# Kernel tuning notes

Hardware: AMD Instinct MI355X
Metric: run time of the kernel (lower is better)

The kernel has to match this reference:

```python
import jax, jax.numpy as jnp
import numpy as np

B, L, H, S = 16, 2048, 1024, 32
P, N_ASP, N_RAT = 256, 8, 5


def _layernorm(x, scale, bias, eps=1e-5):
    mu = jnp.mean(x, axis=-1, keepdims=True)
    var = jnp.mean(jnp.square(x - mu), axis=-1, keepdims=True)
    return (x - mu) * jax.lax.rsqrt(var + eps) * scale + bias


def _bndl(x, ln_s, ln_b, W):
    # BnDropLin eval: LayerNorm -> (Dropout off) -> Linear(no bias)
    return _layernorm(x, ln_s, ln_b) @ W


def setup_inputs() -> dict:
    key = jax.random.key(0)
    ks = jax.random.split(key, 8)
    outputs = jax.random.normal(ks[0], (B, L, H), dtype=jnp.float32)
    mask = jnp.ones((B, L), dtype=jnp.float32)
    # p_index: binary sentence-boundary markers, exactly S per doc, min gap 2
    rng = np.random.default_rng(0)
    p = np.zeros((B, L), dtype=np.int32)
    for b in range(B):
        idx = np.sort(rng.choice(L // 2 - 1, size=S, replace=False)) * 2 + 1
        p[b, idx] = 1
    p_index = jnp.asarray(p)
    sc = 0.02
    params = dict(
        ln_a_s=jnp.ones((H,), jnp.float32), ln_a_b=jnp.zeros((H,), jnp.float32),
        W_a=jax.random.normal(ks[1], (H, P), jnp.float32) * sc,
        ln_s_s=jnp.ones((H,), jnp.float32), ln_s_b=jnp.zeros((H,), jnp.float32),
        W_s=jax.random.normal(ks[2], (H, P), jnp.float32) * sc,
        ln_asp_s=jnp.ones((P,), jnp.float32), ln_asp_b=jnp.zeros((P,), jnp.float32),
        W_asp=jax.random.normal(ks[3], (P, N_ASP + 1), jnp.float32) * sc,
        ln_se_s=jnp.ones((P,), jnp.float32), ln_se_b=jnp.zeros((P,), jnp.float32),
        W_se=jax.random.normal(ks[4], (P, N_RAT), jnp.float32) * sc,
    )
    return dict(outputs=outputs, mask=mask, p_index=p_index, n_sent=S, **params)


def _segment_means(proj, end, start):
    # proj: [B, L, P]; start/end: [B, S] token index ranges [start, end)
    c = jnp.concatenate([jnp.zeros_like(proj[:, :1]), jnp.cumsum(proj, axis=1)], axis=1)  # [B,L+1,P]
    s_end = jnp.take_along_axis(c, end[:, :, None], axis=1)
    s_beg = jnp.take_along_axis(c, start[:, :, None], axis=1)
    cnt = (end - start).astype(proj.dtype)[:, :, None]
    return (s_end - s_beg) / cnt  # [B, S, P]


def reference(outputs, mask, p_index, n_sent,
              ln_a_s, ln_a_b, W_a, ln_s_s, ln_s_b, W_s,
              ln_asp_s, ln_asp_b, W_asp, ln_se_s, ln_se_b, W_se):
    b, l, h = outputs.shape
    n_asp = W_asp.shape[1] - 1
    flat = outputs.reshape(-1, h)
    a_proj = jax.nn.gelu(_bndl(flat, ln_a_s, ln_a_b, W_a), approximate=False).reshape(b, l, -1)
    s_proj = jax.nn.gelu(_bndl(flat, ln_s_s, ln_s_b, W_s), approximate=False).reshape(b, l, -1)
    # sentence boundaries: positions of nonzeros (exactly n_sent per row)
    pos = jnp.where(p_index > 0, jnp.arange(l)[None, :], l)
    pi = jnp.sort(pos, axis=1)[:, :n_sent]                      # [B,S] boundary idx (exclusive end)
    start = jnp.concatenate([jnp.zeros_like(pi[:, :1]), pi[:, :-1] + 1], axis=1)
    a_sent = _segment_means(a_proj, pi, start)                  # [B,S,P]
    s_sent = _segment_means(s_proj, pi, start)                  # [B,S,P]
    a_flat = a_sent.reshape(b * n_sent, -1)
    s_flat = s_sent.reshape(b * n_sent, -1)
    aspect_dist = jax.nn.softmax(_bndl(a_flat, ln_asp_s, ln_asp_b, W_asp), axis=1)  # [N, n_asp+1]
    aw = aspect_dist[:, :n_asp]                                 # [N, n_asp]
    sent_bmm = aw[:, :, None] * s_flat[:, None, :]              # [N, n_asp, P]
    doc_sum = sent_bmm.reshape(b, n_sent, n_asp, -1).sum(axis=1)        # [B, n_asp, P]
    w_sum = aw.reshape(b, n_sent, n_asp).sum(axis=1)[:, :, None]        # [B, n_asp, 1]
    doc_emb = doc_sum / w_sum
    # shared sentiment head (ModuleList([m]*n_asp) aliases one module)
    result = _bndl(doc_emb, ln_se_s, ln_se_b, W_se)             # [B, n_asp, n_rat]
    aspect_doc = aspect_dist.reshape(b, n_sent, n_asp + 1)
    return (result, outputs, aspect_doc)
```

## Files before the change

### kernel.cpp

```cpp
#include <hip/hip_runtime.h>
#include <cstdint>
#include <cstddef>

#define B_   16
#define L_   2048
#define H_   1024
#define S_   32
#define P_   256
#define NASP 8
#define NRAT 5
#define M_   (B_*L_)
#define N_   (2*P_)

typedef unsigned short u16;
typedef __bf16 bf16;
typedef u16  u16x4  __attribute__((ext_vector_type(4)));
typedef u16  u16x8  __attribute__((ext_vector_type(8)));
typedef bf16 bf16x8 __attribute__((ext_vector_type(8)));
typedef float f32x4 __attribute__((ext_vector_type(4)));

__device__ __forceinline__ u16 f2b(float f){
  unsigned int u = __float_as_uint(f);
  u += 0x7FFFu + ((u >> 16) & 1u);
  return (u16)(u >> 16);
}
__device__ __forceinline__ float b2f(u16 v){
  return __uint_as_float(((unsigned int)v) << 16);
}

__device__ __forceinline__ void gload_lds16(const u16* g, u16* l){
  __builtin_amdgcn_global_load_lds(
      (const __attribute__((address_space(1))) unsigned int*)g,
      (__attribute__((address_space(3))) unsigned int*)l, 16, 0, 0);
}

__device__ __forceinline__ float2 block_reduce2(float a, float b){
  __shared__ float sh[8];
  #pragma unroll
  for (int o = 32; o > 0; o >>= 1){
    a += __shfl_down(a, o, 64);
    b += __shfl_down(b, o, 64);
  }
  int w = threadIdx.x >> 6;
  if ((threadIdx.x & 63) == 0){ sh[w] = a; sh[w + 4] = b; }
  __syncthreads();
  float2 r;
  r.x = sh[0] + sh[1] + sh[2] + sh[3];
  r.y = sh[4] + sh[5] + sh[6] + sh[7];
  __syncthreads();
  return r;
}

__global__ void fold_k(const float* __restrict__ Wa, const float* __restrict__ Ws,
                       const float* __restrict__ sa, const float* __restrict__ ba,
                       const float* __restrict__ ss, const float* __restrict__ bs,
                       u16* __restrict__ WcT, float* __restrict__ biasc){
  int n = blockIdx.x;
  const float* W; const float* sc; const float* bi; int col;
  if (n < P_){ W = Wa; sc = sa; bi = ba; col = n; }
  else       { W = Ws; sc = ss; bi = bs; col = n - P_; }
  float bacc = 0.f;
  #pragma unroll
  for (int i = 0; i < 4; ++i){
    int k = threadIdx.x + i * 256;
    float w = W[(size_t)k * P_ + col];
    WcT[(size_t)n * H_ + k] = f2b(w * sc[k]);
    bacc += w * bi[k];
  }
  float2 r = block_reduce2(bacc, 0.f);
  if (threadIdx.x == 0) biasc[n] = r.x;
}

__global__ void markers_k(const int* __restrict__ p_index, int* __restrict__ pi){
  int b = blockIdx.x;
  int lane = threadIdx.x;
  int cnt = 0;
  for (int c = 0; c < L_ / 64; ++c){
    int pos = c * 64 + lane;
    bool f = p_index[(size_t)b * L_ + pos] > 0;
    unsigned long long m = __ballot(f);
    int before = __popcll(m & ((1ull << lane) - 1ull));
    if (f){
      int idx = cnt + before;
      if (idx < S_) pi[b * S_ + idx] = pos;
    }
    cnt += __popcll(m);
  }
}

template<bool FUSE_ECHO>
__global__ void stats_xhat_k(const float* __restrict__ x, u16* __restrict__ xhat,
                             float4* __restrict__ echo){
  int row = blockIdx.x;
  int t = threadIdx.x;
  float4 v = ((const float4*)(x + (size_t)row * H_))[t];
  if (FUSE_ECHO) echo[(size_t)row * (H_ / 4) + t] = v;
  float s  = v.x + v.y + v.z + v.w;
  float ss = v.x*v.x + v.y*v.y + v.z*v.z + v.w*v.w;
  float2 r = block_reduce2(s, ss);
  float mean = r.x * (1.f / H_);
  float var  = fmaxf(r.y * (1.f / H_) - mean * mean, 0.f);
  float rstd = rsqrtf(var + 1e-5f);
  u16x4 o;
  o[0] = f2b((v.x - mean) * rstd);
  o[1] = f2b((v.y - mean) * rstd);
  o[2] = f2b((v.z - mean) * rstd);
  o[3] = f2b((v.w - mean) * rstd);
  ((u16x4*)(xhat + (size_t)row * H_))[t] = o;
}

#define NT_ 16
__global__ __launch_bounds__(512, 2) void gemm_k(const u16* __restrict__ xhat,
                                                 const u16* __restrict__ WcT,
                                                 const float* __restrict__ biasc,
                                                 u16* __restrict__ proj){
  __shared__ __align__(16) u16 As[2][256 * 64];
  __shared__ __align__(16) u16 Bs[2][256 * 64];
  int t = threadIdx.x;
  unsigned int l = blockIdx.x;
  unsigned int xcd  = l & 7;
  unsigned int slot = l >> 3;
  int nbase = (int)(slot & 1) * 256;
  int mbase = (int)(xcd * 16 + (slot >> 1)) * 256;

  int w = t >> 6, lane = t & 63;
  int wr = w >> 2, wc = w & 3;
  int quad = lane >> 4, l15 = lane & 15;

  int rin = lane >> 3;
  int g = (lane & 7) ^ rin;
  const u16* gA[4]; const u16* gB[4]; int off[4];
  #pragma unroll
  for (int i = 0; i < 4; ++i){
    int r = w * 32 + i * 8 + rin;
    gA[i] = xhat + (size_t)(mbase + r) * H_ + g * 8;
    gB[i] = WcT  + (size_t)(nbase + r) * H_ + g * 8;
    off[i] = (w * 4 + i) * 512;
  }

  f32x4 acc[8][4] = {};

#define STAGE_(buf, tile) do{ int kk_ = (tile) * 64;            \
    gload_lds16(gA[0] + kk_, &As[buf][off[0]]);                 \
    gload_lds16(gA[1] + kk_, &As[buf][off[1]]);                 \
    gload_lds16(gA[2] + kk_, &As[buf][off[2]]);                 \
    gload_lds16(gA[3] + kk_, &As[buf][off[3]]);                 \
    gload_lds16(gB[0] + kk_, &Bs[buf][off[0]]);                 \
    gload_lds16(gB[1] + kk_, &Bs[buf][off[1]]);                 \
    gload_lds16(gB[2] + kk_, &Bs[buf][off[2]]);                 \
    gload_lds16(gB[3] + kk_, &Bs[buf][off[3]]);                 \
  }while(0)

  STAGE_(0, 0);
  STAGE_(1, 1);
  asm volatile("s_waitcnt vmcnt(8)" ::: "memory");
  __builtin_amdgcn_sched_barrier(0);
  __builtin_amdgcn_s_barrier();

  for (int kt = 0; kt < NT_; ++kt){
    int cur = kt & 1;
    __builtin_amdgcn_s_setprio(1);
    #pragma unroll
    for (int s = 0; s < 2; ++s){
      bf16x8 af[8], bfr[4];
      #pragma unroll
      for (int im = 0; im < 8; ++im){
        int R = wr * 128 + im * 16 + l15;
        int c = (s * 4 + quad) ^ (R & 7);
        af[im] = *reinterpret_cast<const bf16x8*>(&As[cur][R * 64 + c * 8]);
      }
      #pragma unroll
      for (int in = 0; in < 4; ++in){
        int R = wc * 64 + in * 16 + l15;
        int c = (s * 4 + quad) ^ (R & 7);
        bfr[in] = *reinterpret_cast<const bf16x8*>(&Bs[cur][R * 64 + c * 8]);
      }
      #pragma unroll
      for (int im = 0; im < 8; ++im)
        #pragma unroll
        for (int in = 0; in < 4; ++in)
          acc[im][in] = __builtin_amdgcn_mfma_f32_16x16x32_bf16(af[im], bfr[in], acc[im][in], 0, 0, 0);
    }
    __builtin_amdgcn_s_setprio(0);
    if (kt == NT_ - 1) break;
    __builtin_amdgcn_s_barrier();
    if (kt + 2 < NT_){
      STAGE_(cur, kt + 2);
      asm volatile("s_waitcnt vmcnt(8)" ::: "memory");
    } else {
      asm volatile("s_waitcnt vmcnt(0)" ::: "memory");
    }
    __builtin_amdgcn_sched_barrier(0);
    __builtin_amdgcn_s_barrier();
  }
#undef STAGE_

  #pragma unroll
  for (int in = 0; in < 4; ++in){
    int col = nbase + wc * 64 + in * 16 + l15;
    float bv = biasc[col];
    #pragma unroll
    for (int im = 0; im < 8; ++im){
      #pragma unroll
      for (int r = 0; r < 4; ++r){
        int rowg = mbase + wr * 128 + im * 16 + quad * 4 + r;
        float vv = acc[im][in][r] + bv;
        float gl = 0.5f * vv * (1.0f + erff(vv * 0.70710678118654752f));
        proj[(size_t)rowg * N_ + col] = f2b(gl);
      }
    }
  }
}

__global__ __launch_bounds__(1024) void segmean_k(const u16* __restrict__ proj,
                                                  const int* __restrict__ pi,
                                                  float* __restrict__ sent){
  int b = blockIdx.x, j = blockIdx.y;
  int t = threadIdx.x;
  int rg   = t >> 6;
  int lane = t & 63;
  int end   = pi[b * S_ + j];
  int start = (j == 0) ? 0 : (pi[b * S_ + j - 1] + 1);
  end   = min(max(end, 0), L_);
  start = min(max(start, 0), end);
  int cnt = max(end - start, 1);
  float inv = 1.0f / (float)cnt;

  float s[8] = {};
  const u16* base = proj + ((size_t)b * L_ + start) * N_ + lane * 8;
  for (int r = rg; r < cnt; r += 16){
    u16x8 v = *reinterpret_cast<const u16x8*>(base + (size_t)r * N_);
    #pragma unroll
    for (int k = 0; k < 8; ++k) s[k] += b2f(v[k]);
  }

  __shared__ float sh[16][N_];
  #pragma unroll
  for (int k = 0; k < 8; ++k) sh[rg][lane * 8 + k] = s[k];
  __syncthreads();

  if (t < N_){
    float acc = 0.f;
    #pragma unroll
    for (int g = 0; g < 16; ++g) acc += sh[g][t];
    sent[((size_t)b * S_ + j) * N_ + t] = acc * inv;
  }
}

__global__ void aspect_k(const float* __restrict__ sent,
                         const float* __restrict__ lns, const float* __restrict__ lnb,
                         const float* __restrict__ Wasp,
                         float* __restrict__ out_adoc, float* __restrict__ aw){
  int sidx = blockIdx.x;
  int t = threadIdx.x;
  float a = sent[(size_t)sidx * N_ + t];
  float2 r = block_reduce2(a, a * a);
  float mean = r.x * (1.f / P_);
  float var  = fmaxf(r.y * (1.f / P_) - mean * mean, 0.f);
  float rstd = rsqrtf(var + 1e-5f);
  __shared__ float shv[P_];
  shv[t] = (a - mean) * rstd * lns[t] + lnb[t];
  __syncthreads();
  __shared__ float lg[NASP + 1];
  if (t < NASP + 1){
    float acc = 0.f;
    for (int p = 0; p < P_; ++p) acc += shv[p] * Wasp[p * (NASP + 1) + t];
    lg[t] = acc;
  }
  __syncthreads();
  __shared__ float pr[NASP + 1];
  if (t == 0){
    float m = lg[0];
    #pragma unroll
    for (int i = 1; i < NASP + 1; ++i) m = fmaxf(m, lg[i]);
    float s = 0.f;
    #pragma unroll
    for (int i = 0; i < NASP + 1; ++i){ float e = expf(lg[i] - m); pr[i] = e; s += e; }
    float is = 1.f / s;
    #pragma unroll
    for (int i = 0; i < NASP + 1; ++i) pr[i] *= is;
  }
  __syncthreads();
  if (t < NASP + 1) out_adoc[(size_t)sidx * (NASP + 1) + t] = pr[t];
  if (t < NASP)     aw[(size_t)sidx * NASP + t] = pr[t];
}

__global__ void result_k(const float* __restrict__ sent, const float* __restrict__ aw,
                         const float* __restrict__ lns, const float* __restrict__ lnb,
                         const float* __restrict__ Wse, float* __restrict__ out){
  int ba = blockIdx.x;
  int b = ba >> 3, a = ba & 7;
  int t = threadIdx.x;
  float acc = 0.f, wsum = 0.f;
  for (int s2 = 0; s2 < S_; ++s2){
    float w = aw[((size_t)(b * S_ + s2)) * NASP + a];
    acc  += w * sent[((size_t)(b * S_ + s2)) * N_ + P_ + t];
    wsum += w;
  }
  float d = acc / fmaxf(wsum, 1e-20f);
  float2 r = block_reduce2(d, d * d);
  float mean = r.x * (1.f / P_);
  float var  = fmaxf(r.y * (1.f / P_) - mean * mean, 0.f);
  float rstd = rsqrtf(var + 1e-5f);
  __shared__ float shv[P_];
  shv[t] = (d - mean) * rstd * lns[t] + lnb[t];
  __syncthreads();
  if (t < NRAT){
    float s = 0.f;
    for (int p = 0; p < P_; ++p) s += shv[p] * Wse[p * NRAT + t];
    out[(size_t)ba * NRAT + t] = s;
  }
}

__global__ void copy_k(const float4* __restrict__ src, float4* __restrict__ dst){
  size_t i = (size_t)blockIdx.x * 256 + threadIdx.x;
  dst[i] = src[i];
}

extern "C" void kernel_launch(void* const* d_in, const int* in_sizes, int n_in,
                              void* d_out, int out_size, void* d_ws, size_t ws_size,
                              hipStream_t stream) {
  const float* x        = (const float*)d_in[0];
  const int*   p_index  = (const int*)d_in[2];
  const float* ln_a_s   = (const float*)d_in[4];
  const float* ln_a_b   = (const float*)d_in[5];
  const float* W_a      = (const float*)d_in[6];
  const float* ln_s_s   = (const float*)d_in[7];
  const float* ln_s_b   = (const float*)d_in[8];
  const float* W_s      = (const float*)d_in[9];
  const float* ln_asp_s = (const float*)d_in[10];
  const float* ln_asp_b = (const float*)d_in[11];
  const float* W_asp    = (const float*)d_in[12];
  const float* ln_se_s  = (const float*)d_in[13];
  const float* ln_se_b  = (const float*)d_in[14];
  const float* W_se     = (const float*)d_in[15];

  float* out_result = (float*)d_out;
  float* out_echo   = out_result + 640;
  float* out_adoc   = out_echo + (size_t)M_ * H_;

  char* ws = (char*)d_ws;
  u16*   WcT   = (u16*)ws;   ws += (size_t)N_ * H_ * 2;
  float* biasc = (float*)ws; ws += (size_t)N_ * 4;
  int*   pi    = (int*)ws;   ws += (size_t)B_ * S_ * 4;
  float* sent  = (float*)ws; ws += (size_t)B_ * S_ * N_ * 4;
  float* aw    = (float*)ws; ws += (size_t)B_ * S_ * NASP * 4;

  size_t small_used = (size_t)(ws - (char*)d_ws);
  size_t big_need   = small_used + (size_t)M_ * N_ * 2 + (size_t)M_ * H_ * 2;
  bool   big_ws     = ws_size >= big_need;

  u16* proj; u16* xhat;
  if (big_ws){
    proj = (u16*)ws;
    xhat = proj + (size_t)M_ * N_;
  } else {
    proj = (u16*)out_echo;
    xhat = proj + (size_t)M_ * N_;
  }

  fold_k<<<N_, 256, 0, stream>>>(W_a, W_s, ln_a_s, ln_a_b, ln_s_s, ln_s_b, WcT, biasc);
  markers_k<<<B_, 64, 0, stream>>>(p_index, pi);
  if (big_ws)
    stats_xhat_k<true ><<<M_, 256, 0, stream>>>(x, xhat, (float4*)out_echo);
  else
    stats_xhat_k<false><<<M_, 256, 0, stream>>>(x, xhat, nullptr);
  gemm_k<<<256, 512, 0, stream>>>(xhat, WcT, biasc, proj);
  segmean_k<<<dim3(B_, S_), 1024, 0, stream>>>(proj, pi, sent);
  aspect_k<<<B_ * S_, 256, 0, stream>>>(sent, ln_asp_s, ln_asp_b, W_asp, out_adoc, aw);
  result_k<<<B_ * NASP, 256, 0, stream>>>(sent, aw, ln_se_s, ln_se_b, W_se, out_result);
  if (!big_ws)
    copy_k<<<(M_ * H_ / 4) / 256, 256, 0, stream>>>((const float4*)x, (float4*)out_echo);
}
```

Before: 393.5 us.

## Restructure GEMM main loop into four barrier-synced phases with interleaved prefetch

The GEMM k-loop now prefetches only one tile ahead instead of two. The global-to-LDS loads are split into four chunks, each issued alongside one of four LDS-read/MFMA phases, with block barriers between phases. The aim is to spread memory traffic evenly and keep the waves in lockstep, in the style of ping-pong scheduling. The s_setprio calls are dropped. Separately, the xhat and WcT stores are switched to nontemporal stores. The extra barriers and the shallower prefetch may expose more latency.

```diff
diff --git a/kernel.cpp b/kernel.cpp
--- a/kernel.cpp
+++ b/kernel.cpp
@@ -64,7 +64,7 @@
   for (int i = 0; i < 4; ++i){
     int k = threadIdx.x + i * 256;
     float w = W[(size_t)k * P_ + col];
-    WcT[(size_t)n * H_ + k] = f2b(w * sc[k]);
+    __builtin_nontemporal_store(f2b(w * sc[k]), &WcT[(size_t)n * H_ + k]);
     bacc += w * bi[k];
   }
   float2 r = block_reduce2(bacc, 0.f);
@@ -106,7 +106,7 @@
   o[1] = f2b((v.y - mean) * rstd);
   o[2] = f2b((v.z - mean) * rstd);
   o[3] = f2b((v.w - mean) * rstd);
-  ((u16x4*)(xhat + (size_t)row * H_))[t] = o;
+  __builtin_nontemporal_store(o, (u16x4*)(xhat + (size_t)row * H_) + t);
 }
 
 #define NT_ 16
@@ -140,60 +140,76 @@
 
   f32x4 acc[8][4] = {};
 
-#define STAGE_(buf, tile) do{ int kk_ = (tile) * 64;            \
-    gload_lds16(gA[0] + kk_, &As[buf][off[0]]);                 \
-    gload_lds16(gA[1] + kk_, &As[buf][off[1]]);                 \
-    gload_lds16(gA[2] + kk_, &As[buf][off[2]]);                 \
-    gload_lds16(gA[3] + kk_, &As[buf][off[3]]);                 \
-    gload_lds16(gB[0] + kk_, &Bs[buf][off[0]]);                 \
-    gload_lds16(gB[1] + kk_, &Bs[buf][off[1]]);                 \
-    gload_lds16(gB[2] + kk_, &Bs[buf][off[2]]);                 \
-    gload_lds16(gB[3] + kk_, &Bs[buf][off[3]]);                 \
-  }while(0)
-
-  STAGE_(0, 0);
-  STAGE_(1, 1);
-  asm volatile("s_waitcnt vmcnt(8)" ::: "memory");
+  #pragma unroll
+  for (int i = 0; i < 4; ++i){
+    gload_lds16(gA[i], &As[0][off[i]]);
+    gload_lds16(gB[i], &Bs[0][off[i]]);
+  }
+  asm volatile("s_waitcnt vmcnt(0)" ::: "memory");
   __builtin_amdgcn_sched_barrier(0);
   __builtin_amdgcn_s_barrier();
 
+#define LDA8(dst, S, IM) { int R_ = wr*128 + (IM)*16 + l15;                  \
+    int c_ = ((S)*4+quad) ^ (R_ & 7);                                        \
+    dst = *reinterpret_cast<const bf16x8*>(&As[cur][R_*64 + c_*8]); }
+#define LDB8(dst, S, IN) { int R_ = wc*64 + (IN)*16 + l15;                   \
+    int c_ = ((S)*4+quad) ^ (R_ & 7);                                        \
+    dst = *reinterpret_cast<const bf16x8*>(&Bs[cur][R_*64 + c_*8]); }
+#define PHASE_WAIT  __builtin_amdgcn_s_barrier();                            \
+    asm volatile("s_waitcnt lgkmcnt(0)" ::: "memory");                       \
+    __builtin_amdgcn_sched_barrier(0);
+#define MM4(AV, I)                                                           \
+    acc[I][0] = __builtin_amdgcn_mfma_f32_16x16x32_bf16(AV, b0, acc[I][0], 0,0,0); \
+    acc[I][1] = __builtin_amdgcn_mfma_f32_16x16x32_bf16(AV, b1, acc[I][1], 0,0,0); \
+    acc[I][2] = __builtin_amdgcn_mfma_f32_16x16x32_bf16(AV, b2, acc[I][2], 0,0,0); \
+    acc[I][3] = __builtin_amdgcn_mfma_f32_16x16x32_bf16(AV, b3, acc[I][3], 0,0,0);
+
   for (int kt = 0; kt < NT_; ++kt){
-    int cur = kt & 1;
-    __builtin_amdgcn_s_setprio(1);
-    #pragma unroll
-    for (int s = 0; s < 2; ++s){
-      bf16x8 af[8], bfr[4];
-      #pragma unroll
-      for (int im = 0; im < 8; ++im){
-        int R = wr * 128 + im * 16 + l15;
-        int c = (s * 4 + quad) ^ (R & 7);
-        af[im] = *reinterpret_cast<const bf16x8*>(&As[cur][R * 64 + c * 8]);
-      }
-      #pragma unroll
-      for (int in = 0; in < 4; ++in){
-        int R = wc * 64 + in * 16 + l15;
-        int c = (s * 4 + quad) ^ (R & 7);
-        bfr[in] = *reinterpret_cast<const bf16x8*>(&Bs[cur][R * 64 + c * 8]);
-      }
-      #pragma unroll
-      for (int im = 0; im < 8; ++im)
-        #pragma unroll
-        for (int in = 0; in < 4; ++in)
-          acc[im][in] = __builtin_amdgcn_mfma_f32_16x16x32_bf16(af[im], bfr[in], acc[im][in], 0, 0, 0);
+    int cur = kt & 1, nxt = cur ^ 1;
+    int kk1 = (kt + 1) * 64;
+    bool pf = (kt + 1 < NT_);
+    bf16x8 a0, a1, a2, a3, b0, b1, b2, b3;
+
+    LDB8(b0,0,0); LDB8(b1,0,1); LDB8(b2,0,2); LDB8(b3,0,3);
+    LDA8(a0,0,0); LDA8(a1,0,1); LDA8(a2,0,2); LDA8(a3,0,3);
+    if (pf){ gload_lds16(gA[0]+kk1, &As[nxt][off[0]]);
+             gload_lds16(gA[1]+kk1, &As[nxt][off[1]]); }
+    PHASE_WAIT;
+    MM4(a0,0) MM4(a1,1) MM4(a2,2) MM4(a3,3)
+    __builtin_amdgcn_s_barrier();
+
+    LDA8(a0,0,4); LDA8(a1,0,5); LDA8(a2,0,6); LDA8(a3,0,7);
+    if (pf){ gload_lds16(gA[2]+kk1, &As[nxt][off[2]]);
+             gload_lds16(gA[3]+kk1, &As[nxt][off[3]]); }
+    PHASE_WAIT;
+    MM4(a0,4) MM4(a1,5) MM4(a2,6) MM4(a3,7)
+    __builtin_amdgcn_s_barrier();
+
+    LDB8(b0,1,0); LDB8(b1,1,1); LDB8(b2,1,2); LDB8(b3,1,3);
+    LDA8(a0,1,0); LDA8(a1,1,1); LDA8(a2,1,2); LDA8(a3,1,3);
+    if (pf){ gload_lds16(gB[0]+kk1, &Bs[nxt][off[0]]);
+             gload_lds16(gB[1]+kk1, &Bs[nxt][off[1]]); }
+    PHASE_WAIT;
+    MM4(a0,0) MM4(a1,1) MM4(a2,2) MM4(a3,3)
+    __builtin_amdgcn_s_barrier();
+
+    LDA8(a0,1,4); LDA8(a1,1,5); LDA8(a2,1,6); LDA8(a3,1,7);
+    if (pf){ gload_lds16(gB[2]+kk1, &Bs[nxt][off[2]]);
+             gload_lds16(gB[3]+kk1, &Bs[nxt][off[3]]); }
+    PHASE_WAIT;
+    MM4(a0,4) MM4(a1,5) MM4(a2,6) MM4(a3,7)
+    __builtin_amdgcn_s_barrier();
+
+    if (pf){
+      asm volatile("s_waitcnt vmcnt(0)" ::: "memory");
+      __builtin_amdgcn_sched_barrier(0);
+      __builtin_amdgcn_s_barrier();
     }
-    __builtin_amdgcn_s_setprio(0);
-    if (kt == NT_ - 1) break;
-    __builtin_amdgcn_s_barrier();
-    if (kt + 2 < NT_){
-      STAGE_(cur, kt + 2);
-      asm volatile("s_waitcnt vmcnt(8)" ::: "memory");
-    } else {
-      asm volatile("s_waitcnt vmcnt(0)" ::: "memory");
-    }
-    __builtin_amdgcn_sched_barrier(0);
-    __builtin_amdgcn_s_barrier();
-  }
-#undef STAGE_
+  }
+#undef LDA8
+#undef LDB8
+#undef PHASE_WAIT
+#undef MM4
 
   #pragma unroll
   for (int in = 0; in < 4; ++in){
```

Result: no change. 396.2 us (+0.7%).
